# Kernel tuning notes

Measured on AMD Instinct MI355X. Metric: run time of the kernel, lower is better.

## Reference

```python
import jax, jax.numpy as jnp
import numpy as np

N_NODES = 40000
N_EDGES = 320000
IN_C = 256
OUT_C = 256
K = 5


def setup_inputs() -> dict:
    key = jax.random.key(0)
    k1, k2, k3, k4, k5 = jax.random.split(key, 5)
    x = jax.random.normal(k1, (N_NODES, IN_C), dtype=jnp.float32)
    edge_index = jax.random.randint(k2, (2, N_EDGES), 0, N_NODES, dtype=jnp.int64)
    edge_weight = jax.random.uniform(k3, (N_EDGES,), dtype=jnp.float32)
    # parameters: uniform(-stdv, stdv) with stdv = 1/sqrt(in_channels * K)
    stdv = 1.0 / np.sqrt(IN_C * K)
    weight = jax.random.uniform(k4, (K, IN_C, OUT_C), dtype=jnp.float32,
                                minval=-stdv, maxval=stdv)
    bias = jax.random.uniform(k5, (OUT_C,), dtype=jnp.float32,
                              minval=-stdv, maxval=stdv)
    return {"x": x, "edge_index": edge_index, "edge_weight": edge_weight,
            "weight": weight, "bias": bias}


def reference(x, edge_index, edge_weight, weight, bias):
    row, col = edge_index[0], edge_index[1]
    num_nodes = x.shape[0]
    k_order = weight.shape[0]

    # remove_self_loops: mask out row==col edges (static-shape equivalent)
    keep = (row != col)
    ew = jnp.where(keep, edge_weight, 0.0)

    # degree over rows (counting only non-self-loop edges), D^{-1/2}
    deg = jax.ops.segment_sum(keep.astype(x.dtype), row, num_segments=num_nodes)
    deg_inv_sqrt = jnp.where(deg > 0, jax.lax.rsqrt(jnp.maximum(deg, 1.0)), 0.0)

    # scaled Laplacian edge values: -d_r^{-1/2} * w * d_c^{-1/2}
    lap = -deg_inv_sqrt[row] * ew * deg_inv_sqrt[col]

    def spmm(v):  # [N, C] -> [N, C] : scatter-add of lap-weighted gathered rows
        return jax.ops.segment_sum(lap[:, None] * v[col], row, num_segments=num_nodes)

    # Chebyshev recursion: T0 = x, T1 = L x, T_k = 2 L T_{k-1} - T_{k-2}
    tx0 = x
    out = tx0 @ weight[0]
    if k_order > 1:
        tx1 = spmm(x)
        out = out + tx1 @ weight[1]
        for k in range(2, k_order):
            tx2 = 2.0 * spmm(tx1) - tx0
            out = out + tx2 @ weight[k]
            tx0, tx1 = tx1, tx2
    return out + bias
```

## Files before the change

kernel.cpp:

```cpp
#include <hip/hip_runtime.h>

#define NN 40000
#define NE 320000
#define C 256
#define KORD 5
#define KT 1280
#define ELLW 40

typedef __attribute__((ext_vector_type(8))) short short8;
typedef __attribute__((ext_vector_type(4))) float floatx4;
typedef unsigned short bf16_t;
typedef unsigned long long u64;

__device__ __forceinline__ bf16_t f2bf(float f) {
    union { float f; unsigned u; } v; v.f = f;
    unsigned r = v.u + 0x7fffu + ((v.u >> 16) & 1u);
    return (bf16_t)(r >> 16);
}
__device__ __forceinline__ float bf2f(bf16_t h) {
    union { unsigned u; float f; } v; v.u = ((unsigned)h) << 16;
    return v.f;
}

#define GLL16(gsrc, ldst)                                                        \
    __builtin_amdgcn_global_load_lds(                                            \
        (const __attribute__((address_space(1))) void*)(gsrc),                   \
        (__attribute__((address_space(3))) void*)(ldst), 16, 0, 0)

__global__ __launch_bounds__(256)
void mega0_kernel(const int* __restrict__ ei,
                  int* __restrict__ self, int* __restrict__ cntA,
                  const float* __restrict__ x, bf16_t* __restrict__ abf,
                  const float* __restrict__ W, bf16_t* __restrict__ WT) {
    int bid = blockIdx.x, t = threadIdx.x;
    if (bid < 1250) {
        int e = bid * 256 + t;
        int r = ei[e];
        int c = ei[NE + e];
        atomicAdd(&cntA[r], 1);
        if (r == c) atomicAdd(&self[r], 1);
    } else if (bid < 11250) {
        int i = (bid - 1250) * 256 + t;
        int n = i >> 6, cg = i & 63;
        float4 f = *(const float4*)&x[(size_t)n * C + cg * 4];
        ushort4 h;
        h.x = f2bf(f.x); h.y = f2bf(f.y); h.z = f2bf(f.z); h.w = f2bf(f.w);
        *(ushort4*)&abf[(size_t)n * KT + cg * 4] = h;
    } else {
        int i = (bid - 11250) * 256 + t;
        int n = i & 255, kt = i >> 8;
        WT[(size_t)n * KT + kt] = f2bf(W[(size_t)kt * 256 + n]);
    }
}

__global__ __launch_bounds__(256)
void fill_kernel(const int* __restrict__ ei,
                 const float* __restrict__ ew,
                 const int* __restrict__ self,
                 const int* __restrict__ cntA,
                 int* __restrict__ cur,
                 u64* __restrict__ ell) {
    int e = blockIdx.x * 256 + threadIdx.x;
    if (e >= NE) return;
    int r = ei[e];
    int c = ei[NE + e];
    int pos = atomicAdd(&cur[r], 1);
    float w = (r != c) ? ew[e] : 0.0f;
    int dgr = cntA[r] - self[r];
    int dgc = cntA[c] - self[c];
    float dr = (dgr > 0) ? rsqrtf((float)dgr) : 0.0f;
    float dc = (dgc > 0) ? rsqrtf((float)dgc) : 0.0f;
    float v = -dr * w * dc;
    union { float f; unsigned u; } vb; vb.f = v;
    ell[(size_t)r * ELLW + pos] = ((u64)vb.u << 32) | (unsigned)c;
}

__global__ __launch_bounds__(256)
void spmm_kernel(const bf16_t* __restrict__ Vb,
                 const bf16_t* __restrict__ subb,
                 const int* __restrict__ cntA,
                 const u64* __restrict__ ell,
                 bf16_t* __restrict__ outb,
                 float alpha, int use_sub) {
    int wave = __builtin_amdgcn_readfirstlane(threadIdx.x >> 6);
    int lane = threadIdx.x & 63;
    int n = blockIdx.x * 4 + wave;
    const u64* row = ell + (size_t)n * ELLW;
    int jmax = (cntA[n] + 7) & ~7;
    int cb = lane * 4;
    float a0 = 0.f, a1 = 0.f, a2 = 0.f, a3 = 0.f;
    for (int j = 0; j < jmax; j += 8) {
        u64 pp[8]; ushort4 vv[8];
#pragma unroll
        for (int u = 0; u < 8; ++u) pp[u] = row[j + u];
#pragma unroll
        for (int u = 0; u < 8; ++u)
            vv[u] = *(const ushort4*)&Vb[(size_t)(unsigned)(pp[u] & 0xffffffffu) * KT + cb];
#pragma unroll
        for (int u = 0; u < 8; ++u) {
            union { unsigned u; float f; } wb; wb.u = (unsigned)(pp[u] >> 32);
            float w = wb.f;
            a0 += w * bf2f(vv[u].x); a1 += w * bf2f(vv[u].y);
            a2 += w * bf2f(vv[u].z); a3 += w * bf2f(vv[u].w);
        }
    }
    float r0, r1, r2, r3;
    if (use_sub) {
        ushort4 s = *(const ushort4*)&subb[(size_t)n * KT + cb];
        r0 = alpha * a0 - bf2f(s.x);
        r1 = alpha * a1 - bf2f(s.y);
        r2 = alpha * a2 - bf2f(s.z);
        r3 = alpha * a3 - bf2f(s.w);
    } else {
        r0 = alpha * a0; r1 = alpha * a1; r2 = alpha * a2; r3 = alpha * a3;
    }
    ushort4 h;
    h.x = f2bf(r0); h.y = f2bf(r1); h.z = f2bf(r2); h.w = f2bf(r3);
    *(ushort4*)&outb[(size_t)n * KT + cb] = h;
}

__global__ __launch_bounds__(256, 2)
void gemm_mfma(const bf16_t* __restrict__ Abf,
               const bf16_t* __restrict__ WT,
               const float* __restrict__ bias,
               float* __restrict__ out) {
    __shared__ bf16_t smem[3][12288];
    int tid = threadIdx.x;
    int w = tid >> 6, lane = tid & 63;
    int m0 = blockIdx.x * 64;
    int n0 = blockIdx.y * 128;
    int wm = w & 1, wn = w >> 1;
    int quad = lane >> 4, l16 = lane & 15, l7 = l16 & 7;

    const bf16_t* srcbase[6];
#pragma unroll
    for (int j = 0; j < 6; ++j) {
        int gi = (w * 6 + j) * 64 + lane;
        int isB = gi >= 512;
        int t  = isB ? gi - 512 : gi;
        int row = t >> 3;
        int pg = t & 7;
        int g  = pg ^ (row & 7);
        srcbase[j] = (isB ? WT + (size_t)(n0 + row) * KT
                          : Abf + (size_t)(m0 + row) * KT) + g * 8;
    }

    int arowb = wm * 32 + l16;
    int browb = wn * 64 + l16;

    floatx4 acc[2][4] = {};

    const int NT = KT / 64;

#pragma unroll
    for (int j = 0; j < 6; ++j)
        GLL16(srcbase[j] + 0 * 64, &smem[0][(w * 6 + j) * 512]);
#pragma unroll
    for (int j = 0; j < 6; ++j)
        GLL16(srcbase[j] + 1 * 64, &smem[1][(w * 6 + j) * 512]);

    int bufc = 0;
    for (int t = 0; t < NT; ++t) {
        if (t < NT - 1) {
            asm volatile("s_waitcnt vmcnt(6)" ::: "memory");
        } else {
            asm volatile("s_waitcnt vmcnt(0)" ::: "memory");
        }
        __builtin_amdgcn_sched_barrier(0);
        __builtin_amdgcn_s_barrier();

        if (t + 2 < NT) {
            int bnext = bufc + 2; if (bnext >= 3) bnext -= 3;
#pragma unroll
            for (int j = 0; j < 6; ++j)
                GLL16(srcbase[j] + (t + 2) * 64, &smem[bnext][(w * 6 + j) * 512]);
        }

        const bf16_t* sb = smem[bufc];
#pragma unroll
        for (int c = 0; c < 2; ++c) {
            int gp   = (c * 4 + quad) ^ l7;
            int aoff = (arowb * 8 + gp) * 8;
            int boff = 4096 + (browb * 8 + gp) * 8;
            short8 af[2], bfr[4];
#pragma unroll
            for (int mt = 0; mt < 2; ++mt) af[mt]  = *(const short8*)&sb[aoff + mt * 1024];
#pragma unroll
            for (int nt = 0; nt < 4; ++nt) bfr[nt] = *(const short8*)&sb[boff + nt * 1024];
#pragma unroll
            for (int mt = 0; mt < 2; ++mt)
#pragma unroll
                for (int nt = 0; nt < 4; ++nt)
                    acc[mt][nt] = __builtin_amdgcn_mfma_f32_16x16x32_bf16(
                        af[mt], bfr[nt], acc[mt][nt], 0, 0, 0);
        }

        bufc += 1; if (bufc == 3) bufc = 0;
    }

#pragma unroll
    for (int nt = 0; nt < 4; ++nt) {
        int n = n0 + wn * 64 + nt * 16 + l16;
        float bv = bias[n];
#pragma unroll
        for (int mt = 0; mt < 2; ++mt) {
            int mbase = m0 + wm * 32 + mt * 16 + quad * 4;
#pragma unroll
            for (int r = 0; r < 4; ++r)
                out[(size_t)(mbase + r) * C + n] = acc[mt][nt][r] + bv;
        }
    }
}


extern "C" void kernel_launch(void* const* d_in, const int* in_sizes, int n_in,
                              void* d_out, int out_size, void* d_ws, size_t ws_size,
                              hipStream_t stream) {
    const float* x    = (const float*)d_in[0];
    const int*   ei   = (const int*)d_in[1];
    const float* ew   = (const float*)d_in[2];
    const float* W    = (const float*)d_in[3];
    const float* bias = (const float*)d_in[4];
    float* out = (float*)d_out;

    char* p = (char*)d_ws;
    auto carve = [&](size_t bytes) {
        char* q = p;
        p += (bytes + 255) & ~(size_t)255;
        return q;
    };
    int*    self    = (int*)   carve(NN * 4);
    int*    cntA    = (int*)   carve(NN * 4);
    int*    cur     = (int*)   carve(NN * 4);
    u64*    ell     = (u64*)   carve((size_t)NN * ELLW * 8);
    bf16_t* abf     = (bf16_t*)carve((size_t)NN * KT * 2);
    bf16_t* WT      = (bf16_t*)carve((size_t)C * KT * 2);
    (void)ws_size; (void)n_in; (void)in_sizes; (void)out_size;

    const int NB_E = (NE + 255) / 256;

    hipMemsetAsync(self, 0, (size_t)NN * 4 * 3 + (size_t)NN * ELLW * 8, stream);

    mega0_kernel<<<12530, 256, 0, stream>>>(ei, self, cntA, x, abf, W, WT);

    fill_kernel<<<NB_E, 256, 0, stream>>>(ei, ew, self, cntA, cur, ell);

    spmm_kernel<<<NN / 4, 256, 0, stream>>>(abf + 0 * 256, nullptr, cntA, ell,
                                            abf + 1 * 256, 1.0f, 0);
    spmm_kernel<<<NN / 4, 256, 0, stream>>>(abf + 1 * 256, abf + 0 * 256, cntA, ell,
                                            abf + 2 * 256, 2.0f, 1);
    spmm_kernel<<<NN / 4, 256, 0, stream>>>(abf + 2 * 256, abf + 1 * 256, cntA, ell,
                                            abf + 3 * 256, 2.0f, 1);
    spmm_kernel<<<NN / 4, 256, 0, stream>>>(abf + 3 * 256, abf + 2 * 256, cntA, ell,
                                            abf + 4 * 256, 2.0f, 1);

    dim3 ggrid(625, 2);
    gemm_mfma<<<ggrid, 256, 0, stream>>>(abf, WT, bias, out);
}
```

Before: 278.7 us.

## Fuse ELL fill and four SpMM passes into one persistent kernel with grid barriers

Replaces the fill kernel and four separate SpMM launches with a single persistent kernel of 512 blocks x 1024 threads. Stages are separated by a software grid-wide barrier built on atomics, and rows are distributed across waves with a grid-stride loop. The aim is to cut four kernel launch gaps and tail effects. In exchange it relies on all 512 blocks being co-resident, otherwise it deadlocks, and it adds barrier spin cost and possibly lower occupancy from the 1024-thread blocks.

```diff
diff --git a/kernel.cpp b/kernel.cpp
--- a/kernel.cpp
+++ b/kernel.cpp
@@ -6,6 +6,10 @@
 #define KORD 5
 #define KT 1280
 #define ELLW 40
+
+#define PBLK 512
+#define PTHR 1024
+#define PWAVES (PBLK * (PTHR / 64))
 
 typedef __attribute__((ext_vector_type(8))) short short8;
 typedef __attribute__((ext_vector_type(4))) float floatx4;
@@ -53,38 +57,28 @@
     }
 }
 
-__global__ __launch_bounds__(256)
-void fill_kernel(const int* __restrict__ ei,
-                 const float* __restrict__ ew,
-                 const int* __restrict__ self,
-                 const int* __restrict__ cntA,
-                 int* __restrict__ cur,
-                 u64* __restrict__ ell) {
-    int e = blockIdx.x * 256 + threadIdx.x;
-    if (e >= NE) return;
-    int r = ei[e];
-    int c = ei[NE + e];
-    int pos = atomicAdd(&cur[r], 1);
-    float w = (r != c) ? ew[e] : 0.0f;
-    int dgr = cntA[r] - self[r];
-    int dgc = cntA[c] - self[c];
-    float dr = (dgr > 0) ? rsqrtf((float)dgr) : 0.0f;
-    float dc = (dgc > 0) ? rsqrtf((float)dgc) : 0.0f;
-    float v = -dr * w * dc;
-    union { float f; unsigned u; } vb; vb.f = v;
-    ell[(size_t)r * ELLW + pos] = ((u64)vb.u << 32) | (unsigned)c;
-}
-
-__global__ __launch_bounds__(256)
-void spmm_kernel(const bf16_t* __restrict__ Vb,
-                 const bf16_t* __restrict__ subb,
-                 const int* __restrict__ cntA,
-                 const u64* __restrict__ ell,
-                 bf16_t* __restrict__ outb,
-                 float alpha, int use_sub) {
-    int wave = __builtin_amdgcn_readfirstlane(threadIdx.x >> 6);
-    int lane = threadIdx.x & 63;
-    int n = blockIdx.x * 4 + wave;
+__device__ __forceinline__ void grid_sync(unsigned* bar) {
+    __syncthreads();
+    if (threadIdx.x == 0) {
+        unsigned g = __hip_atomic_load(&bar[0], __ATOMIC_ACQUIRE, __HIP_MEMORY_SCOPE_AGENT);
+        unsigned a = __hip_atomic_fetch_add(&bar[32], 1u, __ATOMIC_ACQ_REL, __HIP_MEMORY_SCOPE_AGENT);
+        if (a == PBLK - 1) {
+            __hip_atomic_store(&bar[32], 0u, __ATOMIC_RELAXED, __HIP_MEMORY_SCOPE_AGENT);
+            __hip_atomic_store(&bar[0], g + 1u, __ATOMIC_RELEASE, __HIP_MEMORY_SCOPE_AGENT);
+        } else {
+            while (__hip_atomic_load(&bar[0], __ATOMIC_ACQUIRE, __HIP_MEMORY_SCOPE_AGENT) == g)
+                __builtin_amdgcn_s_sleep(2);
+        }
+    }
+    __syncthreads();
+}
+
+__device__ __forceinline__ void spmm_row(const bf16_t* __restrict__ Vb,
+                                         const bf16_t* __restrict__ subb,
+                                         const int* __restrict__ cntA,
+                                         const u64* __restrict__ ell,
+                                         bf16_t* __restrict__ outb,
+                                         int n, int lane, float alpha, int use_sub) {
     const u64* row = ell + (size_t)n * ELLW;
     int jmax = (cntA[n] + 7) & ~7;
     int cb = lane * 4;
@@ -117,6 +111,49 @@
     ushort4 h;
     h.x = f2bf(r0); h.y = f2bf(r1); h.z = f2bf(r2); h.w = f2bf(r3);
     *(ushort4*)&outb[(size_t)n * KT + cb] = h;
+}
+
+__global__ __launch_bounds__(PTHR, 8)
+void spmm4p_kernel(const int* __restrict__ ei,
+                   const float* __restrict__ ew,
+                   const int* __restrict__ self,
+                   const int* __restrict__ cntA,
+                   int* __restrict__ cur,
+                   u64* __restrict__ ell,
+                   bf16_t* __restrict__ abf,
+                   unsigned* __restrict__ bar) {
+    {
+        int e = blockIdx.x * PTHR + threadIdx.x;
+        if (e < NE) {
+            int r = ei[e];
+            int c = ei[NE + e];
+            int pos = atomicAdd(&cur[r], 1);
+            float w = (r != c) ? ew[e] : 0.0f;
+            int dgr = cntA[r] - self[r];
+            int dgc = cntA[c] - self[c];
+            float dr = (dgr > 0) ? rsqrtf((float)dgr) : 0.0f;
+            float dc = (dgc > 0) ? rsqrtf((float)dgc) : 0.0f;
+            float v = -dr * w * dc;
+            union { float f; unsigned u; } vb; vb.f = v;
+            ell[(size_t)r * ELLW + pos] = ((u64)vb.u << 32) | (unsigned)c;
+        }
+    }
+    grid_sync(bar);
+
+    int lane = threadIdx.x & 63;
+    int gw = blockIdx.x * (PTHR / 64) + (threadIdx.x >> 6);
+
+    for (int n = gw; n < NN; n += PWAVES)
+        spmm_row(abf + 0 * 256, nullptr, cntA, ell, abf + 1 * 256, n, lane, 1.0f, 0);
+    grid_sync(bar);
+    for (int n = gw; n < NN; n += PWAVES)
+        spmm_row(abf + 1 * 256, abf + 0 * 256, cntA, ell, abf + 2 * 256, n, lane, 2.0f, 1);
+    grid_sync(bar);
+    for (int n = gw; n < NN; n += PWAVES)
+        spmm_row(abf + 2 * 256, abf + 1 * 256, cntA, ell, abf + 3 * 256, n, lane, 2.0f, 1);
+    grid_sync(bar);
+    for (int n = gw; n < NN; n += PWAVES)
+        spmm_row(abf + 3 * 256, abf + 2 * 256, cntA, ell, abf + 4 * 256, n, lane, 2.0f, 1);
 }
 
 __global__ __launch_bounds__(256, 2)
@@ -229,30 +266,20 @@
         p += (bytes + 255) & ~(size_t)255;
         return q;
     };
-    int*    self    = (int*)   carve(NN * 4);
-    int*    cntA    = (int*)   carve(NN * 4);
-    int*    cur     = (int*)   carve(NN * 4);
-    u64*    ell     = (u64*)   carve((size_t)NN * ELLW * 8);
-    bf16_t* abf     = (bf16_t*)carve((size_t)NN * KT * 2);
-    bf16_t* WT      = (bf16_t*)carve((size_t)C * KT * 2);
+    int*      self = (int*)     carve(NN * 4);
+    int*      cntA = (int*)     carve(NN * 4);
+    int*      cur  = (int*)     carve(NN * 4);
+    unsigned* bar  = (unsigned*)carve(256);
+    u64*      ell  = (u64*)     carve((size_t)NN * ELLW * 8);
+    bf16_t*   abf  = (bf16_t*)  carve((size_t)NN * KT * 2);
+    bf16_t*   WT   = (bf16_t*)  carve((size_t)C * KT * 2);
     (void)ws_size; (void)n_in; (void)in_sizes; (void)out_size;
 
-    const int NB_E = (NE + 255) / 256;
-
-    hipMemsetAsync(self, 0, (size_t)NN * 4 * 3 + (size_t)NN * ELLW * 8, stream);
+    hipMemsetAsync(self, 0, (size_t)NN * 4 * 3 + 256 + (size_t)NN * ELLW * 8, stream);
 
     mega0_kernel<<<12530, 256, 0, stream>>>(ei, self, cntA, x, abf, W, WT);
 
-    fill_kernel<<<NB_E, 256, 0, stream>>>(ei, ew, self, cntA, cur, ell);
-
-    spmm_kernel<<<NN / 4, 256, 0, stream>>>(abf + 0 * 256, nullptr, cntA, ell,
-                                            abf + 1 * 256, 1.0f, 0);
-    spmm_kernel<<<NN / 4, 256, 0, stream>>>(abf + 1 * 256, abf + 0 * 256, cntA, ell,
-                                            abf + 2 * 256, 2.0f, 1);
-    spmm_kernel<<<NN / 4, 256, 0, stream>>>(abf + 2 * 256, abf + 1 * 256, cntA, ell,
-                                            abf + 3 * 256, 2.0f, 1);
-    spmm_kernel<<<NN / 4, 256, 0, stream>>>(abf + 3 * 256, abf + 2 * 256, cntA, ell,
-                                            abf + 4 * 256, 2.0f, 1);
+    spmm4p_kernel<<<PBLK, PTHR, 0, stream>>>(ei, ew, self, cntA, cur, ell, abf, bar);
 
     dim3 ggrid(625, 2);
     gemm_mfma<<<ggrid, 256, 0, stream>>>(abf, WT, bias, out);
```

Result: slower. 626.4 us (+124.8%).
